# Kernel optimization log

Hardware: AMD Instinct MI355X
Metric: run time of the kernel (lower is better)

Reference implementation:

```python
import jax, jax.numpy as jnp
import numpy as np

B, S, D, DFF, H, V, L = 2, 1024, 1024, 4096, 16, 32000, 8
DH = D // H
EPS = 1e-5

def _pe():
    pos = np.arange(S, dtype=np.float32)[:, None]
    div = np.exp(np.arange(0, D, 2, dtype=np.float32) * (-np.log(10000.0) / D))
    pe = np.zeros((S, D), dtype=np.float32)
    pe[:, 0::2] = np.sin(pos * div)
    pe[:, 1::2] = np.cos(pos * div)
    return jnp.asarray(pe)

PE = _pe()

def _ln(h, g, b):
    m = jnp.mean(h, axis=-1, keepdims=True)
    v = jnp.mean((h - m) ** 2, axis=-1, keepdims=True)
    return (h - m) * jax.lax.rsqrt(v + EPS) * g + b

def setup_inputs():
    key = jax.random.key(0)
    k = jax.random.split(key, 16)
    sc = 0.02
    return {
        'x': jax.random.randint(k[0], (B, S), 0, V),
        'mask': jnp.tril(jnp.ones((1, 1, S, S), dtype=bool)),
        'emb': jax.random.normal(k[1], (V, D)) * sc,
        'Wq': jax.random.normal(k[2], (L, D, D)) * sc,
        'Wk': jax.random.normal(k[3], (L, D, D)) * sc,
        'Wv': jax.random.normal(k[4], (L, D, D)) * sc,
        'Wo': jax.random.normal(k[5], (L, D, D)) * sc,
        'ln1_g': jnp.ones((L, D)), 'ln1_b': jnp.zeros((L, D)),
        'ln2_g': jnp.ones((L, D)), 'ln2_b': jnp.zeros((L, D)),
        'W1': jax.random.normal(k[6], (L, D, DFF)) * sc,
        'b1': jnp.zeros((L, DFF)),
        'W2': jax.random.normal(k[7], (L, DFF, D)) * sc,
        'b2': jnp.zeros((L, D)),
        'lnf_g': jnp.ones((D,)), 'lnf_b': jnp.zeros((D,)),
        'projW': jax.random.normal(k[8], (D, V)) * sc,
        'projb': jnp.zeros((V,)),
    }

def reference(x, mask, emb, Wq, Wk, Wv, Wo, ln1_g, ln1_b, ln2_g, ln2_b,
              W1, b1, W2, b2, lnf_g, lnf_b, projW, projb):
    # embedding * sqrt(D) + positional encoding
    h = emb[x] * jnp.sqrt(jnp.float32(D)) + PE[None, :, :]
    scale = 1.0 / jnp.sqrt(jnp.float32(DH))
    for i in range(L):
        # --- self-attention sublayer (pre-LN residual) ---
        a_in = _ln(h, ln1_g[i], ln1_b[i])
        q = (a_in @ Wq[i]).reshape(B, S, H, DH)
        kk = (a_in @ Wk[i]).reshape(B, S, H, DH)
        v = (a_in @ Wv[i]).reshape(B, S, H, DH)
        scores = jnp.einsum('bqhd,bkhd->bhqk', q, kk) * scale
        scores = jnp.where(mask, scores, -1e9)
        attn = jax.nn.softmax(scores, axis=-1)
        o = jnp.einsum('bhqk,bkhd->bqhd', attn, v).reshape(B, S, D)
        h = h + o @ Wo[i]
        # --- feed-forward sublayer ---
        f_in = _ln(h, ln2_g[i], ln2_b[i])
        h = h + (jax.nn.relu(f_in @ W1[i] + b1[i]) @ W2[i] + b2[i])
    h = _ln(h, lnf_g, lnf_b)
    return h @ projW + projb
```

## Files before the change

kernel.cpp:

```cpp
#include <hip/hip_runtime.h>

typedef __bf16 bf16;
typedef __bf16 bf16x4 __attribute__((ext_vector_type(4)));
typedef __bf16 bf16x8 __attribute__((ext_vector_type(8)));
typedef float f32x4 __attribute__((ext_vector_type(4)));
typedef short short4v __attribute__((ext_vector_type(4)));

__device__ __forceinline__ short f2bs(float x) {
  bf16 hv = (bf16)x;
  return __builtin_bit_cast(short, hv);
}

__device__ __forceinline__ void gl_lds16(const void* g, void* l) {
  __builtin_amdgcn_global_load_lds(
      (const __attribute__((address_space(1))) unsigned int*)g,
      (__attribute__((address_space(3))) unsigned int*)l, 16, 0, 0);
}

__global__ __launch_bounds__(256) void wt_k(const float* __restrict__ in,
    bf16* __restrict__ out, int K, int N, long in_ls, long out_ls)
{
  __shared__ float t[64][33];
  const int z = blockIdx.z;
  const float* ip = in + (size_t)z * in_ls;
  bf16* op = out + (size_t)z * out_ls;
  const int n0 = blockIdx.x * 32, k0 = blockIdx.y * 64;
  const int tid = threadIdx.x;
  const int kr = tid >> 3, nc = (tid & 7) * 4;
#pragma unroll
  for (int hh = 0; hh < 2; ++hh) {
    float4 v = *(const float4*)(ip + (size_t)(k0 + kr + hh * 32) * N + n0 + nc);
    t[kr + hh * 32][nc]     = v.x;
    t[kr + hh * 32][nc + 1] = v.y;
    t[kr + hh * 32][nc + 2] = v.z;
    t[kr + hh * 32][nc + 3] = v.w;
  }
  __syncthreads();
  const int nr = tid >> 3, kc = (tid & 7) * 8;
  bf16x8 o;
#pragma unroll
  for (int j = 0; j < 8; ++j) o[j] = (bf16)t[kc + j][nr];
  *(bf16x8*)(op + (size_t)(n0 + nr) * K + k0 + kc) = o;
}

__global__ __launch_bounds__(256) void embed_k(const int* __restrict__ x,
    const float* __restrict__ emb, float* __restrict__ h)
{
  const int m = blockIdx.x, t = threadIdx.x;
  const int s = m & 1023;
  const int tok = x[m];
  const int d0 = t * 4;
  float4 e = *(const float4*)(emb + (size_t)tok * 1024 + d0);
  const float* ep = &e.x;
  float r[4];
#pragma unroll
  for (int j = 0; j < 4; ++j) {
    int d = d0 + j;
    float freq = expf((float)(d & ~1) * (-9.2103403719761836f / 1024.f));
    float ang = (float)s * freq;
    float pe = (d & 1) ? cosf(ang) : sinf(ang);
    r[j] = ep[j] * 32.f + pe;
  }
  *(float4*)(h + (size_t)m * 1024 + d0) = make_float4(r[0], r[1], r[2], r[3]);
}

__global__ __launch_bounds__(256) void ln_k(const float* __restrict__ h,
    const float* __restrict__ g, const float* __restrict__ b,
    bf16* __restrict__ out)
{
  const int row = blockIdx.x, t = threadIdx.x;
  const float* hr = h + (size_t)row * 1024;
  float4 x = *(const float4*)(hr + t * 4);
  float s  = x.x + x.y + x.z + x.w;
  float ss = x.x * x.x + x.y * x.y + x.z * x.z + x.w * x.w;
#pragma unroll
  for (int off = 32; off >= 1; off >>= 1) {
    s  += __shfl_down(s, off);
    ss += __shfl_down(ss, off);
  }
  __shared__ float sb[4], ssb[4];
  if ((t & 63) == 0) { sb[t >> 6] = s; ssb[t >> 6] = ss; }
  __syncthreads();
  s  = sb[0] + sb[1] + sb[2] + sb[3];
  ss = ssb[0] + ssb[1] + ssb[2] + ssb[3];
  const float mean = s * (1.f / 1024.f);
  const float var  = ss * (1.f / 1024.f) - mean * mean;
  const float rstd = rsqrtf(var + 1e-5f);
  const float* xp = &x.x;
#pragma unroll
  for (int j = 0; j < 4; ++j) {
    int d = t * 4 + j;
    out[(size_t)row * 1024 + d] = (bf16)((xp[j] - mean) * rstd * g[d] + b[d]);
  }
}

__global__ __launch_bounds__(512, 2) void gemm256_k(
    const bf16* __restrict__ A, const bf16* __restrict__ Bt,
    const float* __restrict__ bias, float* __restrict__ C,
    int M, int N, int K)
{
  __shared__ __align__(16) bf16 As[2][256 * 64];
  __shared__ __align__(16) bf16 Bs[2][256 * 64];

  const int nwg = gridDim.x;
  const int orig = blockIdx.x;
  const int q8 = nwg >> 3, r8 = nwg & 7;
  const int xcd = orig & 7, loc = orig >> 3;
  const int wg = (xcd < r8 ? xcd * (q8 + 1) : r8 * (q8 + 1) + (xcd - r8) * q8) + loc;
  const int nrowt = M >> 8;
  const int rowt = wg & (nrowt - 1);
  const int colt = wg / nrowt;
  const int m0 = rowt * 256;
  const int n0 = colt * 256;
  const int nt = K >> 6;

  const int tid = threadIdx.x;
  const int lane = tid & 63;
  const int wbase = tid & ~63;
  const int wid = tid >> 6;
  const int wm = wid >> 2, wn = wid & 3;
  const int qr = lane & 15, grp = lane >> 4;

  f32x4 acc[8][4];
#pragma unroll
  for (int i = 0; i < 8; ++i)
#pragma unroll
    for (int j = 0; j < 4; ++j) acc[i][j] = (f32x4){0.f, 0.f, 0.f, 0.f};

  auto stageA = [&](int bufi, int kt) {
#pragma unroll
    for (int it = 0; it < 4; ++it) {
      const int idx = it * 512 + tid;
      const int row = idx >> 3, c = idx & 7;
      const int bo = (c * 16) ^ ((row & 7) << 4);
      gl_lds16((const char*)(A + (size_t)(m0 + row) * K + kt) + bo,
               (char*)&As[bufi][0] + (size_t)(it * 512 + wbase) * 16);
    }
  };
  auto stageB = [&](int bufi, int kt) {
#pragma unroll
    for (int it = 0; it < 4; ++it) {
      const int idx = it * 512 + tid;
      const int row = idx >> 3, c = idx & 7;
      const int bo = (c * 16) ^ ((row & 7) << 4);
      gl_lds16((const char*)(Bt + (size_t)(n0 + row) * K + kt) + bo,
               (char*)&Bs[bufi][0] + (size_t)(it * 512 + wbase) * 16);
    }
  };

  stageA(0, 0); stageB(0, 0);
  asm volatile("s_waitcnt vmcnt(0)" ::: "memory");
  __builtin_amdgcn_s_barrier();

  for (int t = 0; t < nt; ++t) {
    const int cur = t & 1;
    const bool pfch = (t + 1 < nt);
    if (pfch) stageA(cur ^ 1, (t + 1) * 64);
#pragma unroll
    for (int ks = 0; ks < 2; ++ks) {
      bf16x8 af[8], bfr[4];
#pragma unroll
      for (int mi = 0; mi < 8; ++mi) {
        const int arow = wm * 128 + mi * 16 + qr;
        const int ab = arow * 128 + ((grp * 16 + ks * 64) ^ ((arow & 7) << 4));
        af[mi] = *(const bf16x8*)((const char*)&As[cur][0] + ab);
      }
#pragma unroll
      for (int ni = 0; ni < 4; ++ni) {
        const int brow = wn * 64 + ni * 16 + qr;
        const int bb = brow * 128 + ((grp * 16 + ks * 64) ^ ((brow & 7) << 4));
        bfr[ni] = *(const bf16x8*)((const char*)&Bs[cur][0] + bb);
      }
      __builtin_amdgcn_s_setprio(1);
#pragma unroll
      for (int mi = 0; mi < 8; ++mi)
#pragma unroll
        for (int ni = 0; ni < 4; ++ni)
          acc[mi][ni] = __builtin_amdgcn_mfma_f32_16x16x32_bf16(
              af[mi], bfr[ni], acc[mi][ni], 0, 0, 0);
      __builtin_amdgcn_s_setprio(0);
      if (ks == 0 && pfch) stageB(cur ^ 1, (t + 1) * 64);
    }
    asm volatile("s_waitcnt vmcnt(0)" ::: "memory");
    __builtin_amdgcn_s_barrier();
  }

#pragma unroll
  for (int ni = 0; ni < 4; ++ni) {
    const int colg = n0 + wn * 64 + ni * 16 + qr;
    const float bv = bias[colg];
#pragma unroll
    for (int mi = 0; mi < 8; ++mi) {
      const int rowg0 = m0 + wm * 128 + mi * 16 + grp * 4;
#pragma unroll
      for (int r = 0; r < 4; ++r)
        C[(size_t)(rowg0 + r) * N + colg] = acc[mi][ni][r] + bv;
    }
  }
}

template<int MODE, int NSPLIT>
__global__ __launch_bounds__(256) void gemm3_k(
    const bf16* __restrict__ A, const bf16* __restrict__ Bt,
    const float* __restrict__ bias, void* __restrict__ Cout,
    float* __restrict__ Hacc, bf16* __restrict__ Vt,
    int M, int N, int K)
{
  __shared__ __align__(16) bf16 As[2][128 * 64];
  __shared__ __align__(16) bf16 Bs[2][128 * 64];

  const int nwg = gridDim.x;
  const int orig = blockIdx.x;
  const int q8 = nwg >> 3, r8 = nwg & 7;
  const int xcd = orig & 7, loc = orig >> 3;
  const int wg = (xcd < r8 ? xcd * (q8 + 1) : r8 * (q8 + 1) + (xcd - r8) * q8) + loc;
  const int nrowt = M >> 7;
  const int ntiles = nrowt * (N >> 7);
  const int split = (NSPLIT > 1) ? (wg / ntiles) : 0;
  const int tile  = (NSPLIT > 1) ? (wg % ntiles) : wg;
  const int rowt = tile & (nrowt - 1);
  const int colt = tile / nrowt;
  const int m0 = rowt * 128;
  const int n0 = colt * 128;
  const int Ks = K / NSPLIT;
  const int k_begin = split * Ks;
  const int nt = Ks >> 6;

  const int tid = threadIdx.x;
  const int lane = tid & 63;
  const int wbase = tid & ~63;
  const int wid = tid >> 6;
  const int wm = wid >> 1, wn = wid & 1;
  const int qr = lane & 15, grp = lane >> 4;

  f32x4 acc[4][4];
#pragma unroll
  for (int i = 0; i < 4; ++i)
#pragma unroll
    for (int j = 0; j < 4; ++j) acc[i][j] = (f32x4){0.f, 0.f, 0.f, 0.f};

  auto stage = [&](int bufi, int kt) {
#pragma unroll
    for (int it = 0; it < 4; ++it) {
      const int idx = it * 256 + tid;
      const int row = idx >> 3, c = idx & 7;
      const int bo = (c * 16) ^ ((row & 7) << 4);
      gl_lds16((const char*)(A + (size_t)(m0 + row) * K + kt) + bo,
               (char*)&As[bufi][0] + (size_t)(it * 256 + wbase) * 16);
    }
#pragma unroll
    for (int it = 0; it < 4; ++it) {
      const int idx = it * 256 + tid;
      const int row = idx >> 3, c = idx & 7;
      const int bo = (c * 16) ^ ((row & 7) << 4);
      gl_lds16((const char*)(Bt + (size_t)(n0 + row) * K + kt) + bo,
               (char*)&Bs[bufi][0] + (size_t)(it * 256 + wbase) * 16);
    }
  };

  stage(0, k_begin);
  asm volatile("s_waitcnt vmcnt(0)" ::: "memory");
  __builtin_amdgcn_s_barrier();

  for (int t = 0; t < nt; ++t) {
    const int cur = t & 1;
    if (t + 1 < nt) stage(cur ^ 1, k_begin + (t + 1) * 64);
#pragma unroll
    for (int ks = 0; ks < 2; ++ks) {
      bf16x8 af[4], bfr[4];
#pragma unroll
      for (int mi = 0; mi < 4; ++mi) {
        const int arow = wm * 64 + mi * 16 + qr;
        const int ab = arow * 128 + ((grp * 16 + ks * 64) ^ ((arow & 7) << 4));
        af[mi] = *(const bf16x8*)((const char*)&As[cur][0] + ab);
      }
#pragma unroll
      for (int ni = 0; ni < 4; ++ni) {
        const int brow = wn * 64 + ni * 16 + qr;
        const int bb = brow * 128 + ((grp * 16 + ks * 64) ^ ((brow & 7) << 4));
        bfr[ni] = *(const bf16x8*)((const char*)&Bs[cur][0] + bb);
      }
#pragma unroll
      for (int mi = 0; mi < 4; ++mi)
#pragma unroll
        for (int ni = 0; ni < 4; ++ni)
          acc[mi][ni] = __builtin_amdgcn_mfma_f32_16x16x32_bf16(
              af[mi], bfr[ni], acc[mi][ni], 0, 0, 0);
    }
    asm volatile("s_waitcnt vmcnt(0)" ::: "memory");
    __builtin_amdgcn_s_barrier();
  }

  const int sel = (MODE == 5) ? (n0 >> 10) : 0;
#pragma unroll
  for (int ni = 0; ni < 4; ++ni) {
    const int coln = wn * 64 + ni * 16 + qr;
    const int colg = n0 + coln;
    float bv = 0.f;
    if (MODE == 1) bv = bias[colg];
    if (MODE == 3 && split == 0) bv = bias[colg];
#pragma unroll
    for (int mi = 0; mi < 4; ++mi) {
      const int rowg0 = m0 + wm * 64 + mi * 16 + grp * 4;
      if (MODE == 5 && sel == 2) {
        const int b = rowg0 >> 10, s = rowg0 & 1023;
        bf16x4 pv;
#pragma unroll
        for (int r = 0; r < 4; ++r) pv[r] = (bf16)acc[mi][ni][r];
        *(bf16x4*)(Vt + (size_t)b * 1024 * 1024 + (size_t)(colg & 1023) * 1024 + s) = pv;
      } else {
#pragma unroll
        for (int r = 0; r < 4; ++r) {
          const int rowg = rowg0 + r;
          float v = acc[mi][ni][r];
          if (MODE == 1) {
            v += bv; v = v > 0.f ? v : 0.f;
            ((bf16*)Cout)[(size_t)rowg * N + colg] = (bf16)v;
          } else if (MODE == 2) {
            if (NSPLIT > 1) atomicAdd(&Hacc[(size_t)rowg * N + colg], v);
            else            Hacc[(size_t)rowg * N + colg] += v;
          } else if (MODE == 3) {
            if (NSPLIT > 1) atomicAdd(&Hacc[(size_t)rowg * N + colg], v + bv);
            else            Hacc[(size_t)rowg * N + colg] += v + bv;
          } else if (MODE == 5) {
            bf16* cb = (bf16*)Cout + (size_t)sel * 2048 * 1024;
            cb[(size_t)rowg * 1024 + (colg & 1023)] = (bf16)v;
          }
        }
      }
    }
  }
}

__global__ __launch_bounds__(64) void attn_k(const bf16* __restrict__ qm,
    const bf16* __restrict__ km, const bf16* __restrict__ vt,
    bf16* __restrict__ om)
{
  const int lane = threadIdx.x;
  const int qr = lane & 15, g = lane >> 4;
  const int qt = blockIdx.x & 63;
  const int hh = (blockIdx.x >> 6) & 15;
  const int bb = blockIdx.x >> 10;
  const size_t rowb = (size_t)bb * 1024;
  const int hb = hh * 64;

  const bf16* qp = qm + (rowb + qt * 16 + qr) * 1024 + hb + g * 8;
  const bf16x8 qf0 = *(const bf16x8*)qp;
  const bf16x8 qf1 = *(const bf16x8*)(qp + 32);

  float m_run = -1e30f, l_run = 0.f;
  f32x4 oacc[4];
#pragma unroll
  for (int dt = 0; dt < 4; ++dt) oacc[dt] = (f32x4){0.f, 0.f, 0.f, 0.f};

  const int qglob = qt * 16 + qr;
  const bf16* vtb = vt + (size_t)bb * 1024 * 1024;
  const bf16* kbase = km + rowb * 1024 + hb;

  auto tile_step = [&](int kvt, bool masked) {
    const bf16* kp = kbase + (size_t)kvt * 16 * 1024 + qr * 1024 + g * 8;
    bf16x8 kf0 = *(const bf16x8*)kp;
    bf16x8 kf1 = *(const bf16x8*)(kp + 32);
    bf16x4 vf[4];
#pragma unroll
    for (int dt = 0; dt < 4; ++dt)
      vf[dt] = *(const bf16x4*)(vtb + (size_t)(hb + dt * 16 + qr) * 1024 + kvt * 16 + g * 4);
    f32x4 st = (f32x4){0.f, 0.f, 0.f, 0.f};
    st = __builtin_amdgcn_mfma_f32_16x16x32_bf16(kf0, qf0, st, 0, 0, 0);
    st = __builtin_amdgcn_mfma_f32_16x16x32_bf16(kf1, qf1, st, 0, 0, 0);
    float sc[4];
#pragma unroll
    for (int r = 0; r < 4; ++r) {
      sc[r] = st[r] * 0.125f;
      if (masked && (kvt * 16 + g * 4 + r > qglob)) sc[r] = -1e30f;
    }
    float mloc = fmaxf(fmaxf(sc[0], sc[1]), fmaxf(sc[2], sc[3]));
    mloc = fmaxf(mloc, __shfl_xor(mloc, 16));
    mloc = fmaxf(mloc, __shfl_xor(mloc, 32));
    float m_new = fmaxf(m_run, mloc);
    float alpha = __expf(m_run - m_new);
    float p[4], ps = 0.f;
#pragma unroll
    for (int r = 0; r < 4; ++r) { p[r] = __expf(sc[r] - m_new); ps += p[r]; }
    ps += __shfl_xor(ps, 16);
    ps += __shfl_xor(ps, 32);
    l_run = l_run * alpha + ps;
    m_run = m_new;
    short4v pfa;
#pragma unroll
    for (int r = 0; r < 4; ++r) pfa[r] = f2bs(p[r]);
#pragma unroll
    for (int dt = 0; dt < 4; ++dt) {
      oacc[dt] *= alpha;
      oacc[dt] = __builtin_amdgcn_mfma_f32_16x16x16bf16_1k(
          __builtin_bit_cast(short4v, vf[dt]), pfa, oacc[dt], 0, 0, 0);
    }
  };

  const int nun = qt;
  int kvt = 0;
  for (; kvt + 1 < nun; kvt += 2) {
    const bf16* kpa = kbase + (size_t)kvt * 16 * 1024 + qr * 1024 + g * 8;
    const bf16* kpb = kpa + 16 * 1024;
    bf16x8 ka0 = *(const bf16x8*)kpa;
    bf16x8 ka1 = *(const bf16x8*)(kpa + 32);
    bf16x8 kb0 = *(const bf16x8*)kpb;
    bf16x8 kb1 = *(const bf16x8*)(kpb + 32);
    bf16x4 vfa[4], vfb[4];
#pragma unroll
    for (int dt = 0; dt < 4; ++dt) {
      const bf16* vp = vtb + (size_t)(hb + dt * 16 + qr) * 1024 + kvt * 16 + g * 4;
      vfa[dt] = *(const bf16x4*)vp;
      vfb[dt] = *(const bf16x4*)(vp + 16);
    }
    f32x4 sa = (f32x4){0.f, 0.f, 0.f, 0.f};
    f32x4 sb = (f32x4){0.f, 0.f, 0.f, 0.f};
    sa = __builtin_amdgcn_mfma_f32_16x16x32_bf16(ka0, qf0, sa, 0, 0, 0);
    sb = __builtin_amdgcn_mfma_f32_16x16x32_bf16(kb0, qf0, sb, 0, 0, 0);
    sa = __builtin_amdgcn_mfma_f32_16x16x32_bf16(ka1, qf1, sa, 0, 0, 0);
    sb = __builtin_amdgcn_mfma_f32_16x16x32_bf16(kb1, qf1, sb, 0, 0, 0);
    float pa[4], pb[4];
    float mloc = -1e30f;
#pragma unroll
    for (int r = 0; r < 4; ++r) {
      pa[r] = sa[r] * 0.125f; pb[r] = sb[r] * 0.125f;
      mloc = fmaxf(mloc, fmaxf(pa[r], pb[r]));
    }
    mloc = fmaxf(mloc, __shfl_xor(mloc, 16));
    mloc = fmaxf(mloc, __shfl_xor(mloc, 32));
    float m_new = fmaxf(m_run, mloc);
    float alpha = __expf(m_run - m_new);
    float ps = 0.f;
#pragma unroll
    for (int r = 0; r < 4; ++r) {
      pa[r] = __expf(pa[r] - m_new); pb[r] = __expf(pb[r] - m_new);
      ps += pa[r] + pb[r];
    }
    ps += __shfl_xor(ps, 16);
    ps += __shfl_xor(ps, 32);
    l_run = l_run * alpha + ps;
    m_run = m_new;
    short4v pfa, pfb;
#pragma unroll
    for (int r = 0; r < 4; ++r) { pfa[r] = f2bs(pa[r]); pfb[r] = f2bs(pb[r]); }
#pragma unroll
    for (int dt = 0; dt < 4; ++dt) {
      oacc[dt] *= alpha;
      oacc[dt] = __builtin_amdgcn_mfma_f32_16x16x16bf16_1k(
          __builtin_bit_cast(short4v, vfa[dt]), pfa, oacc[dt], 0, 0, 0);
      oacc[dt] = __builtin_amdgcn_mfma_f32_16x16x16bf16_1k(
          __builtin_bit_cast(short4v, vfb[dt]), pfb, oacc[dt], 0, 0, 0);
    }
  }
  for (; kvt < nun; ++kvt) tile_step(kvt, false);
  tile_step(qt, true);

  const float inv = 1.f / l_run;
  bf16* op = om + (rowb + qt * 16 + qr) * 1024 + hb;
#pragma unroll
  for (int dt = 0; dt < 4; ++dt)
#pragma unroll
    for (int r = 0; r < 4; ++r)
      op[dt * 16 + g * 4 + r] = (bf16)(oacc[dt][r] * inv);
}

extern "C" void kernel_launch(void* const* d_in, const int* in_sizes, int n_in,
                              void* d_out, int out_size, void* d_ws, size_t ws_size,
                              hipStream_t stream)
{
  (void)in_sizes; (void)n_in; (void)out_size; (void)ws_size;
  const int*   x     = (const int*)d_in[0];
  const float* emb   = (const float*)d_in[2];
  const float* Wq    = (const float*)d_in[3];
  const float* Wk    = (const float*)d_in[4];
  const float* Wv    = (const float*)d_in[5];
  const float* Wo    = (const float*)d_in[6];
  const float* ln1g  = (const float*)d_in[7];
  const float* ln1b  = (const float*)d_in[8];
  const float* ln2g  = (const float*)d_in[9];
  const float* ln2b  = (const float*)d_in[10];
  const float* W1    = (const float*)d_in[11];
  const float* b1    = (const float*)d_in[12];
  const float* W2    = (const float*)d_in[13];
  const float* b2    = (const float*)d_in[14];
  const float* lnfg  = (const float*)d_in[15];
  const float* lnfb  = (const float*)d_in[16];
  const float* projW = (const float*)d_in[17];
  const float* projb = (const float*)d_in[18];

  char* ws = (char*)d_ws;
  const size_t MB = 1u << 20;
  float* h    = (float*)(ws + 0);
  bf16*  ain  = (bf16*)(ws + 8 * MB);
  bf16*  qb   = (bf16*)(ws + 12 * MB);
  bf16*  kb   = (bf16*)(ws + 16 * MB);
  bf16*  vtb  = (bf16*)(ws + 20 * MB);
  bf16*  ob   = (bf16*)(ws + 24 * MB);
  bf16*  mid  = (bf16*)(ws + 28 * MB);
  bf16*  Bqkv = (bf16*)(ws + 44 * MB);
  bf16*  Bo   = (bf16*)(ws + 92 * MB);
  bf16*  B1t  = (bf16*)(ws + 108 * MB);
  bf16*  B2t  = (bf16*)(ws + 172 * MB);
  bf16*  Bprj = (bf16*)(ws + 236 * MB);

  const long M1 = 1024 * 1024, M3 = 3 * M1, M4 = 4 * M1;

  wt_k<<<dim3(32, 16, 8),   256, 0, stream>>>(Wq, Bqkv,          1024, 1024, M1, M3);
  wt_k<<<dim3(32, 16, 8),   256, 0, stream>>>(Wk, Bqkv + M1,     1024, 1024, M1, M3);
  wt_k<<<dim3(32, 16, 8),   256, 0, stream>>>(Wv, Bqkv + 2 * M1, 1024, 1024, M1, M3);
  wt_k<<<dim3(32, 16, 8),   256, 0, stream>>>(Wo, Bo,            1024, 1024, M1, M1);
  wt_k<<<dim3(128, 16, 8),  256, 0, stream>>>(W1, B1t,           1024, 4096, M4, M4);
  wt_k<<<dim3(32, 64, 8),   256, 0, stream>>>(W2, B2t,           4096, 1024, M4, M4);
  wt_k<<<dim3(1000, 16, 1), 256, 0, stream>>>(projW, Bprj,       1024, 32000, 0, 0);

  embed_k<<<dim3(2048), 256, 0, stream>>>(x, emb, h);
  for (int i = 0; i < 8; ++i) {
    ln_k<<<dim3(2048), 256, 0, stream>>>(h, ln1g + i * 1024, ln1b + i * 1024, ain);
    gemm3_k<5,1><<<dim3(384), 256, 0, stream>>>(ain, Bqkv + i * M3, nullptr,
                                                qb, nullptr, vtb, 2048, 3072, 1024);
    attn_k<<<dim3(2048), 64, 0, stream>>>(qb, kb, vtb, ob);
    gemm3_k<2,2><<<dim3(256), 256, 0, stream>>>(ob, Bo + i * M1, nullptr,
                                                nullptr, h, nullptr, 2048, 1024, 1024);
    ln_k<<<dim3(2048), 256, 0, stream>>>(h, ln2g + i * 1024, ln2b + i * 1024, ain);
    gemm3_k<1,1><<<dim3(512), 256, 0, stream>>>(ain, B1t + i * M4, b1 + i * 4096,
                                                mid, nullptr, nullptr, 2048, 4096, 1024);
    gemm3_k<3,2><<<dim3(256), 256, 0, stream>>>(mid, B2t + i * M4, b2 + i * 1024,
                                                nullptr, h, nullptr, 2048, 1024, 4096);
  }
  ln_k<<<dim3(2048), 256, 0, stream>>>(h, lnfg, lnfb, ain);
  gemm256_k<<<dim3(1000), 512, 0, stream>>>(ain, Bprj, projb,
                                            (float*)d_out, 2048, 32000, 1024);
}
```

Measured before the change: 2.170 ms.

## Move GEMM waits to loop head, widen projection GEMM to 1024 threads, vectorize stores

The final vocabulary projection GEMM now runs 16 waves of 1024 threads, each wave computing a 64x64 subtile. Its MFMA operands are swapped so each lane holds four consecutive output columns, which lets the epilogue write float4 stores with vector bias loads. In both GEMM kernels the full vmcnt(0) drain at the end of each K step is replaced by a partial wait and barrier at the top of the loop, so the next tile's loads stay in flight while the current one is consumed. gemm3_k also gains setprio around its MFMA block. The risks are higher register pressure and lower occupancy from the 1024-thread block, and a correctness dependence on the exact vmcnt values.

```diff
diff --git a/kernel.cpp b/kernel.cpp
--- a/kernel.cpp
+++ b/kernel.cpp
@@ -94,7 +94,7 @@
   }
 }
 
-__global__ __launch_bounds__(512, 2) void gemm256_k(
+__global__ __launch_bounds__(1024) void gemm256_k(
     const bf16* __restrict__ A, const bf16* __restrict__ Bt,
     const float* __restrict__ bias, float* __restrict__ C,
     int M, int N, int K)
@@ -121,47 +121,48 @@
   const int wm = wid >> 2, wn = wid & 3;
   const int qr = lane & 15, grp = lane >> 4;
 
-  f32x4 acc[8][4];
-#pragma unroll
-  for (int i = 0; i < 8; ++i)
+  f32x4 acc[4][4];
+#pragma unroll
+  for (int i = 0; i < 4; ++i)
 #pragma unroll
     for (int j = 0; j < 4; ++j) acc[i][j] = (f32x4){0.f, 0.f, 0.f, 0.f};
 
-  auto stageA = [&](int bufi, int kt) {
-#pragma unroll
-    for (int it = 0; it < 4; ++it) {
-      const int idx = it * 512 + tid;
+  auto stage = [&](int bufi, int kt) {
+#pragma unroll
+    for (int it = 0; it < 2; ++it) {
+      const int idx = it * 1024 + tid;
       const int row = idx >> 3, c = idx & 7;
       const int bo = (c * 16) ^ ((row & 7) << 4);
       gl_lds16((const char*)(A + (size_t)(m0 + row) * K + kt) + bo,
-               (char*)&As[bufi][0] + (size_t)(it * 512 + wbase) * 16);
-    }
-  };
-  auto stageB = [&](int bufi, int kt) {
-#pragma unroll
-    for (int it = 0; it < 4; ++it) {
-      const int idx = it * 512 + tid;
+               (char*)&As[bufi][0] + (size_t)(it * 1024 + wbase) * 16);
+    }
+#pragma unroll
+    for (int it = 0; it < 2; ++it) {
+      const int idx = it * 1024 + tid;
       const int row = idx >> 3, c = idx & 7;
       const int bo = (c * 16) ^ ((row & 7) << 4);
       gl_lds16((const char*)(Bt + (size_t)(n0 + row) * K + kt) + bo,
-               (char*)&Bs[bufi][0] + (size_t)(it * 512 + wbase) * 16);
+               (char*)&Bs[bufi][0] + (size_t)(it * 1024 + wbase) * 16);
     }
   };
 
-  stageA(0, 0); stageB(0, 0);
-  asm volatile("s_waitcnt vmcnt(0)" ::: "memory");
-  __builtin_amdgcn_s_barrier();
-
+  stage(0, 0);
   for (int t = 0; t < nt; ++t) {
     const int cur = t & 1;
-    const bool pfch = (t + 1 < nt);
-    if (pfch) stageA(cur ^ 1, (t + 1) * 64);
+    if (t + 1 < nt) {
+      stage(cur ^ 1, (t + 1) * 64);
+      asm volatile("s_waitcnt vmcnt(4)" ::: "memory");
+    } else {
+      asm volatile("s_waitcnt vmcnt(0)" ::: "memory");
+    }
+    __builtin_amdgcn_s_barrier();
+    asm volatile("" ::: "memory");
 #pragma unroll
     for (int ks = 0; ks < 2; ++ks) {
-      bf16x8 af[8], bfr[4];
-#pragma unroll
-      for (int mi = 0; mi < 8; ++mi) {
-        const int arow = wm * 128 + mi * 16 + qr;
+      bf16x8 af[4], bfr[4];
+#pragma unroll
+      for (int mi = 0; mi < 4; ++mi) {
+        const int arow = wm * 64 + mi * 16 + qr;
         const int ab = arow * 128 + ((grp * 16 + ks * 64) ^ ((arow & 7) << 4));
         af[mi] = *(const bf16x8*)((const char*)&As[cur][0] + ab);
       }
@@ -173,28 +174,30 @@
       }
       __builtin_amdgcn_s_setprio(1);
 #pragma unroll
-      for (int mi = 0; mi < 8; ++mi)
+      for (int mi = 0; mi < 4; ++mi)
 #pragma unroll
         for (int ni = 0; ni < 4; ++ni)
           acc[mi][ni] = __builtin_amdgcn_mfma_f32_16x16x32_bf16(
-              af[mi], bfr[ni], acc[mi][ni], 0, 0, 0);
+              bfr[ni], af[mi], acc[mi][ni], 0, 0, 0);
       __builtin_amdgcn_s_setprio(0);
-      if (ks == 0 && pfch) stageB(cur ^ 1, (t + 1) * 64);
-    }
-    asm volatile("s_waitcnt vmcnt(0)" ::: "memory");
+    }
     __builtin_amdgcn_s_barrier();
-  }
-
-#pragma unroll
-  for (int ni = 0; ni < 4; ++ni) {
-    const int colg = n0 + wn * 64 + ni * 16 + qr;
-    const float bv = bias[colg];
-#pragma unroll
-    for (int mi = 0; mi < 8; ++mi) {
-      const int rowg0 = m0 + wm * 128 + mi * 16 + grp * 4;
-#pragma unroll
-      for (int r = 0; r < 4; ++r)
-        C[(size_t)(rowg0 + r) * N + colg] = acc[mi][ni][r] + bv;
+    asm volatile("" ::: "memory");
+  }
+
+#pragma unroll
+  for (int mi = 0; mi < 4; ++mi) {
+    const int rowg = m0 + wm * 64 + mi * 16 + qr;
+#pragma unroll
+    for (int ni = 0; ni < 4; ++ni) {
+      const int colg = n0 + wn * 64 + ni * 16 + grp * 4;
+      float4 bv = *(const float4*)(bias + colg);
+      float4 o;
+      o.x = acc[mi][ni][0] + bv.x;
+      o.y = acc[mi][ni][1] + bv.y;
+      o.z = acc[mi][ni][2] + bv.z;
+      o.w = acc[mi][ni][3] + bv.w;
+      *(float4*)(C + (size_t)rowg * N + colg) = o;
     }
   }
 }
@@ -259,12 +262,16 @@
   };
 
   stage(0, k_begin);
-  asm volatile("s_waitcnt vmcnt(0)" ::: "memory");
-  __builtin_amdgcn_s_barrier();
-
   for (int t = 0; t < nt; ++t) {
     const int cur = t & 1;
-    if (t + 1 < nt) stage(cur ^ 1, k_begin + (t + 1) * 64);
+    if (t + 1 < nt) {
+      stage(cur ^ 1, k_begin + (t + 1) * 64);
+      asm volatile("s_waitcnt vmcnt(8)" ::: "memory");
+    } else {
+      asm volatile("s_waitcnt vmcnt(0)" ::: "memory");
+    }
+    __builtin_amdgcn_s_barrier();
+    asm volatile("" ::: "memory");
 #pragma unroll
     for (int ks = 0; ks < 2; ++ks) {
       bf16x8 af[4], bfr[4];
@@ -280,15 +287,17 @@
         const int bb = brow * 128 + ((grp * 16 + ks * 64) ^ ((brow & 7) << 4));
         bfr[ni] = *(const bf16x8*)((const char*)&Bs[cur][0] + bb);
       }
+      __builtin_amdgcn_s_setprio(1);
 #pragma unroll
       for (int mi = 0; mi < 4; ++mi)
 #pragma unroll
         for (int ni = 0; ni < 4; ++ni)
           acc[mi][ni] = __builtin_amdgcn_mfma_f32_16x16x32_bf16(
               af[mi], bfr[ni], acc[mi][ni], 0, 0, 0);
-    }
-    asm volatile("s_waitcnt vmcnt(0)" ::: "memory");
+      __builtin_amdgcn_s_setprio(0);
+    }
     __builtin_amdgcn_s_barrier();
+    asm volatile("" ::: "memory");
   }
 
   const int sel = (MODE == 5) ? (n0 >> 10) : 0;
@@ -528,6 +537,6 @@
                                                 nullptr, h, nullptr, 2048, 1024, 4096);
   }
   ln_k<<<dim3(2048), 256, 0, stream>>>(h, lnfg, lnfb, ain);
-  gemm256_k<<<dim3(1000), 512, 0, stream>>>(ain, Bprj, projb,
-                                            (float*)d_out, 2048, 32000, 1024);
-}
+  gemm256_k<<<dim3(1000), 1024, 0, stream>>>(ain, Bprj, projb,
+                                             (float*)d_out, 2048, 32000, 1024);
+}
```

After: 2.149 ms. About the same (-1.0%).
